# Performance work log

Measured on AMD Instinct MI355X. Metric: run time of the kernel, lower is better.

The kernel has to match this reference:

```python
import jax, jax.numpy as jnp
import numpy as np

N_VOXELS = 200000
DIM = 96
KVOL = 343  # 7^3 depthwise kernel offsets
N_EDGES = 3200000


def setup_inputs() -> dict:
    key = jax.random.key(0)
    ks = jax.random.split(key, 10)
    feats = jax.random.normal(ks[0], (N_VOXELS, DIM), dtype=jnp.float32)
    w_dw = jax.random.normal(ks[1], (KVOL, DIM), dtype=jnp.float32) * 0.02
    b_dw = jax.random.normal(ks[2], (DIM,), dtype=jnp.float32) * 0.02
    ln_w = jnp.ones((DIM,), dtype=jnp.float32)
    ln_b = jnp.zeros((DIM,), dtype=jnp.float32)
    w1 = jax.random.normal(ks[3], (DIM, 4 * DIM), dtype=jnp.float32) * 0.02
    b1 = jax.random.normal(ks[4], (4 * DIM,), dtype=jnp.float32) * 0.02
    w2 = jax.random.normal(ks[5], (4 * DIM, DIM), dtype=jnp.float32) * 0.02
    b2 = jax.random.normal(ks[6], (DIM,), dtype=jnp.float32) * 0.02
    in_idx = jax.random.randint(ks[7], (N_EDGES,), 0, N_VOXELS, dtype=jnp.int32)
    out_idx = jax.random.randint(ks[8], (N_EDGES,), 0, N_VOXELS, dtype=jnp.int32)
    kernel_idx = jax.random.randint(ks[9], (N_EDGES,), 0, KVOL, dtype=jnp.int32)
    return {"feats": feats, "w_dw": w_dw, "b_dw": b_dw, "ln_w": ln_w,
            "ln_b": ln_b, "w1": w1, "b1": b1, "w2": w2, "b2": b2,
            "in_idx": in_idx, "out_idx": out_idx, "kernel_idx": kernel_idx}


def reference(feats, w_dw, b_dw, ln_w, ln_b, w1, b1, w2, b2,
              in_idx, out_idx, kernel_idx):
    n = feats.shape[0]
    # sparse depthwise conv via kernel-map gather/scatter:
    # out[o, c] += feats[i, c] * w_dw[k, c] for each edge (i, o, k)
    contrib = feats[in_idx] * w_dw[kernel_idx]           # [E, C]
    x = jax.ops.segment_sum(contrib, out_idx, num_segments=n) + b_dw
    # LayerNorm over channels, eps=1e-6
    mu = jnp.mean(x, axis=-1, keepdims=True)
    var = jnp.mean(jnp.square(x - mu), axis=-1, keepdims=True)
    x = (x - mu) * jax.lax.rsqrt(var + 1e-6) * ln_w + ln_b
    # pointwise MLP with exact GELU
    h = jax.nn.gelu(x @ w1 + b1, approximate=False)      # [N, 4C]
    x = h @ w2 + b2                                      # [N, C]
    # residual (drop_path rate 0.0 -> identity)
    return feats + x
```

## Files before the change

kernel.cpp:

```cpp
#include <hip/hip_runtime.h>
#include <hip/hip_bf16.h>

#define NVOX 200000
#define DIM 96
#define KVOL 343
#define NEDGE 3200000
#define HID 384
#define TM 32
#define SLOT_CAP 64

typedef __attribute__((ext_vector_type(8))) __bf16 bf16x8;
typedef __attribute__((ext_vector_type(4))) __bf16 bf16x4;
typedef __attribute__((ext_vector_type(4))) float f32x4;

__global__ void prep(const float* __restrict__ feats, const float* __restrict__ w1,
                     const float* __restrict__ w2, const float* __restrict__ w_dw,
                     __bf16* __restrict__ featsb, __hip_bfloat16* __restrict__ w1t,
                     __hip_bfloat16* __restrict__ w2t, __bf16* __restrict__ wdwb,
                     int* __restrict__ cnt) {
    int t = blockIdx.x * 256 + threadIdx.x;
    float4 v = *(const float4*)(feats + t * 4);
    bf16x4 o;
    o[0] = (__bf16)v.x; o[1] = (__bf16)v.y; o[2] = (__bf16)v.z; o[3] = (__bf16)v.w;
    *(bf16x4*)(featsb + t * 4) = o;
    if (t < HID * DIM) {
        int n1 = t / DIM, k1 = t % DIM;
        w1t[t] = __float2bfloat16(w1[k1 * HID + n1]);
        int n2 = t / HID, k2 = t % HID;
        w2t[t] = __float2bfloat16(w2[k2 * DIM + n2]);
        if (t < KVOL * DIM) wdwb[t] = (__bf16)w_dw[t];
    }
    if (t < NVOX) cnt[t] = 0;
}

__global__ void scatter_slots(const int4* __restrict__ in4, const int4* __restrict__ out4,
                              const int4* __restrict__ k4, int* __restrict__ cnt,
                              unsigned* __restrict__ slots) {
    int t = blockIdx.x * 256 + threadIdx.x;
    int4 i = in4[t], o = out4[t], k = k4[t];
    int d;
    d = atomicAdd(&cnt[o.x], 1);
    __builtin_nontemporal_store((unsigned)i.x | ((unsigned)k.x << 18), &slots[o.x * SLOT_CAP + d]);
    d = atomicAdd(&cnt[o.y], 1);
    __builtin_nontemporal_store((unsigned)i.y | ((unsigned)k.y << 18), &slots[o.y * SLOT_CAP + d]);
    d = atomicAdd(&cnt[o.z], 1);
    __builtin_nontemporal_store((unsigned)i.z | ((unsigned)k.z << 18), &slots[o.z * SLOT_CAP + d]);
    d = atomicAdd(&cnt[o.w], 1);
    __builtin_nontemporal_store((unsigned)i.w | ((unsigned)k.w << 18), &slots[o.w * SLOT_CAP + d]);
}

__global__ __launch_bounds__(256, 4) void fused_all(
    const __bf16* __restrict__ featsb, const __bf16* __restrict__ wdwb,
    const float* __restrict__ b_dw,
    const float* __restrict__ ln_w, const float* __restrict__ ln_b,
    const __hip_bfloat16* __restrict__ w1t, const float* __restrict__ b1,
    const __hip_bfloat16* __restrict__ w2t, const float* __restrict__ b2,
    const unsigned* __restrict__ slots, const int* __restrict__ cnt,
    float* __restrict__ out)
{
    __shared__ __hip_bfloat16 At[TM][104];
    __shared__ __align__(16) char shb[TM * 392 * 2];
    __hip_bfloat16 (*Ht)[392] = (__hip_bfloat16 (*)[392])shb;
    unsigned (*recsL)[68] = (unsigned (*)[68])shb;

    const int t   = threadIdx.x;
    const int blk = blockIdx.x;

    {
        const int row  = t >> 3;
        const int sub  = t & 7;
        const int part = sub & 3;
        const int half = sub >> 2;
        const int c0   = part * 24;
        const int v    = blk * TM + row;

        int c = cnt[v];
        if (c > SLOT_CAP) c = SLOT_CAP;
        const unsigned* sp = slots + v * SLOT_CAP;

        if (sub * 4 < c)
            *(uint4*)&recsL[row][sub * 4] = *(const uint4*)(sp + sub * 4);
        if (32 + sub * 4 < c)
            *(uint4*)&recsL[row][32 + sub * 4] = *(const uint4*)(sp + 32 + sub * 4);
        __syncthreads();

        float xa[24];
        #pragma unroll
        for (int j = 0; j < 24; ++j) xa[j] = 0.f;

        const __bf16* fbase = featsb + c0;
        const __bf16* wbase = wdwb + c0;
        const unsigned* rl = recsL[row];

        const int e_lo = half ? (c >> 1) : 0;
        const int e_hi = half ? c : (c >> 1);

#define LDE(F, W, ee) { unsigned rr = rl[ee]; \
        const __bf16* fr = fbase + (int)(rr & 0x3FFFFu) * DIM; \
        const __bf16* wr = wbase + (int)(rr >> 18) * DIM; \
        F##0 = *(const bf16x8*)(fr);      W##0 = *(const bf16x8*)(wr); \
        F##1 = *(const bf16x8*)(fr + 8);  W##1 = *(const bf16x8*)(wr + 8); \
        F##2 = *(const bf16x8*)(fr + 16); W##2 = *(const bf16x8*)(wr + 16); }

#define ACC(F, W) { \
        _Pragma("unroll") for (int j = 0; j < 8; ++j) xa[j]      += (float)F##0[j] * (float)W##0[j]; \
        _Pragma("unroll") for (int j = 0; j < 8; ++j) xa[8 + j]  += (float)F##1[j] * (float)W##1[j]; \
        _Pragma("unroll") for (int j = 0; j < 8; ++j) xa[16 + j] += (float)F##2[j] * (float)W##2[j]; }

        bf16x8 Af0, Af1, Af2, Aw0, Aw1, Aw2, Bf0, Bf1, Bf2, Bw0, Bw1, Bw2;
        int e = e_lo;
        if (e + 2 <= e_hi) {
            LDE(Af, Aw, e); LDE(Bf, Bw, e + 1);
            e += 2;
            for (; e + 2 <= e_hi; e += 2) {
                bf16x8 Cf0, Cf1, Cf2, Cw0, Cw1, Cw2, Df0, Df1, Df2, Dw0, Dw1, Dw2;
                LDE(Cf, Cw, e); LDE(Df, Dw, e + 1);
                ACC(Af, Aw); ACC(Bf, Bw);
                Af0 = Cf0; Af1 = Cf1; Af2 = Cf2; Aw0 = Cw0; Aw1 = Cw1; Aw2 = Cw2;
                Bf0 = Df0; Bf1 = Df1; Bf2 = Df2; Bw0 = Dw0; Bw1 = Dw1; Bw2 = Dw2;
            }
            ACC(Af, Aw); ACC(Bf, Bw);
        }
        if (e < e_hi) {
            LDE(Af, Aw, e);
            ACC(Af, Aw);
        }
#undef LDE
#undef ACC

        #pragma unroll
        for (int j = 0; j < 24; ++j) xa[j] += __shfl_xor(xa[j], 4);

        float s = 0.f, s2 = 0.f;
        #pragma unroll
        for (int j = 0; j < 24; ++j) {
            float x = xa[j] + b_dw[c0 + j];
            xa[j] = x;
            s += x; s2 += x * x;
        }
        s  += __shfl_xor(s, 1);  s  += __shfl_xor(s, 2);
        s2 += __shfl_xor(s2, 1); s2 += __shfl_xor(s2, 2);
        float mean = s * (1.f / 96.f);
        float var  = s2 * (1.f / 96.f) - mean * mean;
        float rstd = rsqrtf(var + 1e-6f);

        if (half == 0) {
            #pragma unroll
            for (int jj = 0; jj < 3; ++jj) {
                bf16x8 pack;
                #pragma unroll
                for (int j = 0; j < 8; ++j) {
                    int cch = c0 + jj*8 + j;
                    float xn = (xa[jj*8+j] - mean) * rstd * ln_w[cch] + ln_b[cch];
                    pack[j] = (__bf16)xn;
                }
                *(bf16x8*)&At[row][c0 + jj*8] = pack;
            }
        }
    }
    __syncthreads();

    const int w  = t >> 6;
    const int l  = t & 63;
    const int lr = l & 15;
    const int lk = l >> 4;
    const int rb = w >> 1;
    const int jh = w & 1;

    f32x4 acc[12];
    #pragma unroll
    for (int j = 0; j < 12; ++j) acc[j] = (f32x4){0.f, 0.f, 0.f, 0.f};

    #pragma unroll
    for (int kk = 0; kk < 3; ++kk) {
        bf16x8 a = *(const bf16x8*)&At[rb*16 + lr][kk*32 + lk*8];
        #pragma unroll
        for (int j = 0; j < 12; ++j) {
            int col = jh*192 + j*16 + lr;
            bf16x8 b = *(const bf16x8*)&w1t[col * DIM + kk*32 + lk*8];
            acc[j] = __builtin_amdgcn_mfma_f32_16x16x32_bf16(a, b, acc[j], 0, 0, 0);
        }
    }

    #pragma unroll
    for (int j = 0; j < 12; ++j) {
        int col = jh*192 + j*16 + lr;
        float bb = b1[col];
        #pragma unroll
        for (int r = 0; r < 4; ++r) {
            float vv = acc[j][r] + bb;
            float ge = 0.5f * vv * (1.f + erff(vv * 0.70710678f));
            Ht[rb*16 + lk*4 + r][col] = __float2bfloat16(ge);
        }
    }
    __syncthreads();

    f32x4 acc2[3];
    #pragma unroll
    for (int j = 0; j < 3; ++j) acc2[j] = (f32x4){0.f, 0.f, 0.f, 0.f};

    #pragma unroll
    for (int kk = 0; kk < 12; ++kk) {
        bf16x8 a = *(const bf16x8*)&Ht[rb*16 + lr][kk*32 + lk*8];
        #pragma unroll
        for (int j = 0; j < 3; ++j) {
            int col = jh*48 + j*16 + lr;
            bf16x8 b = *(const bf16x8*)&w2t[col * HID + kk*32 + lk*8];
            acc2[j] = __builtin_amdgcn_mfma_f32_16x16x32_bf16(a, b, acc2[j], 0, 0, 0);
        }
    }

    #pragma unroll
    for (int j = 0; j < 3; ++j) {
        int col = jh*48 + j*16 + lr;
        float bb = b2[col];
        #pragma unroll
        for (int r = 0; r < 4; ++r) {
            int grow = blk * TM + rb*16 + lk*4 + r;
            int off = grow * DIM + col;
            float res = (float)featsb[off];
            __builtin_nontemporal_store(acc2[j][r] + bb + res, &out[off]);
        }
    }
}

extern "C" void kernel_launch(void* const* d_in, const int* in_sizes, int n_in,
                              void* d_out, int out_size, void* d_ws, size_t ws_size,
                              hipStream_t stream) {
    const float* feats = (const float*)d_in[0];
    const float* w_dw  = (const float*)d_in[1];
    const float* b_dw  = (const float*)d_in[2];
    const float* ln_w  = (const float*)d_in[3];
    const float* ln_b  = (const float*)d_in[4];
    const float* w1    = (const float*)d_in[5];
    const float* b1    = (const float*)d_in[6];
    const float* w2    = (const float*)d_in[7];
    const float* b2    = (const float*)d_in[8];
    const int* in_idx  = (const int*)d_in[9];
    const int* out_idx = (const int*)d_in[10];
    const int* k_idx   = (const int*)d_in[11];
    float* out = (float*)d_out;

    char* ws = (char*)d_ws;
    unsigned* slots = (unsigned*)ws;
    int* cnt   = (int*)(ws + 51200000);
    __hip_bfloat16* w1t = (__hip_bfloat16*)(ws + 52000000);
    __hip_bfloat16* w2t = (__hip_bfloat16*)(ws + 52073728);
    __bf16* wdwb = (__bf16*)(ws + 52147456);
    __bf16* featsb = (__bf16*)(ws + 52213312);

    prep<<<(NVOX * DIM / 4) / 256, 256, 0, stream>>>(feats, w1, w2, w_dw,
                                                     featsb, w1t, w2t, wdwb, cnt);
    scatter_slots<<<NEDGE / 4 / 256, 256, 0, stream>>>((const int4*)in_idx,
                                                       (const int4*)out_idx,
                                                       (const int4*)k_idx, cnt, slots);
    fused_all<<<NVOX / TM, 256, 0, stream>>>(featsb, wdwb, b_dw, ln_w, ln_b,
                                             w1t, b1, w2t, b2, slots, cnt, out);
}
```

Measured before the change: 535.0 us.

## Use 512 threads per block in fused kernel and split edge gather four ways

```diff
diff --git a/kernel.cpp b/kernel.cpp
--- a/kernel.cpp
+++ b/kernel.cpp
@@ -12,6 +12,7 @@
 typedef __attribute__((ext_vector_type(8))) __bf16 bf16x8;
 typedef __attribute__((ext_vector_type(4))) __bf16 bf16x4;
 typedef __attribute__((ext_vector_type(4))) float f32x4;
+typedef __attribute__((ext_vector_type(4))) int i32x4;
 
 __global__ void prep(const float* __restrict__ feats, const float* __restrict__ w1,
                      const float* __restrict__ w2, const float* __restrict__ w_dw,
@@ -19,10 +20,10 @@
                      __hip_bfloat16* __restrict__ w2t, __bf16* __restrict__ wdwb,
                      int* __restrict__ cnt) {
     int t = blockIdx.x * 256 + threadIdx.x;
-    float4 v = *(const float4*)(feats + t * 4);
+    f32x4 v = __builtin_nontemporal_load((const f32x4*)(feats + t * 4));
     bf16x4 o;
     o[0] = (__bf16)v.x; o[1] = (__bf16)v.y; o[2] = (__bf16)v.z; o[3] = (__bf16)v.w;
-    *(bf16x4*)(featsb + t * 4) = o;
+    __builtin_nontemporal_store(o, (bf16x4*)(featsb + t * 4));
     if (t < HID * DIM) {
         int n1 = t / DIM, k1 = t % DIM;
         w1t[t] = __float2bfloat16(w1[k1 * HID + n1]);
@@ -33,23 +34,30 @@
     if (t < NVOX) cnt[t] = 0;
 }
 
-__global__ void scatter_slots(const int4* __restrict__ in4, const int4* __restrict__ out4,
-                              const int4* __restrict__ k4, int* __restrict__ cnt,
+__global__ void scatter_slots(const i32x4* __restrict__ in4, const i32x4* __restrict__ out4,
+                              const i32x4* __restrict__ k4, int* __restrict__ cnt,
                               unsigned* __restrict__ slots) {
     int t = blockIdx.x * 256 + threadIdx.x;
-    int4 i = in4[t], o = out4[t], k = k4[t];
-    int d;
-    d = atomicAdd(&cnt[o.x], 1);
-    __builtin_nontemporal_store((unsigned)i.x | ((unsigned)k.x << 18), &slots[o.x * SLOT_CAP + d]);
-    d = atomicAdd(&cnt[o.y], 1);
-    __builtin_nontemporal_store((unsigned)i.y | ((unsigned)k.y << 18), &slots[o.y * SLOT_CAP + d]);
-    d = atomicAdd(&cnt[o.z], 1);
-    __builtin_nontemporal_store((unsigned)i.z | ((unsigned)k.z << 18), &slots[o.z * SLOT_CAP + d]);
-    d = atomicAdd(&cnt[o.w], 1);
-    __builtin_nontemporal_store((unsigned)i.w | ((unsigned)k.w << 18), &slots[o.w * SLOT_CAP + d]);
-}
-
-__global__ __launch_bounds__(256, 4) void fused_all(
+    if (t >= NEDGE / 8) return;
+    #pragma unroll
+    for (int h = 0; h < 2; ++h) {
+        int idx = t * 2 + h;
+        i32x4 i = __builtin_nontemporal_load(&in4[idx]);
+        i32x4 o = __builtin_nontemporal_load(&out4[idx]);
+        i32x4 k = __builtin_nontemporal_load(&k4[idx]);
+        int d;
+        d = atomicAdd(&cnt[o.x], 1);
+        __builtin_nontemporal_store((unsigned)i.x | ((unsigned)k.x << 18), &slots[o.x * SLOT_CAP + d]);
+        d = atomicAdd(&cnt[o.y], 1);
+        __builtin_nontemporal_store((unsigned)i.y | ((unsigned)k.y << 18), &slots[o.y * SLOT_CAP + d]);
+        d = atomicAdd(&cnt[o.z], 1);
+        __builtin_nontemporal_store((unsigned)i.z | ((unsigned)k.z << 18), &slots[o.z * SLOT_CAP + d]);
+        d = atomicAdd(&cnt[o.w], 1);
+        __builtin_nontemporal_store((unsigned)i.w | ((unsigned)k.w << 18), &slots[o.w * SLOT_CAP + d]);
+    }
+}
+
+__global__ __launch_bounds__(512, 4) void fused_all(
     const __bf16* __restrict__ featsb, const __bf16* __restrict__ wdwb,
     const float* __restrict__ b_dw,
     const float* __restrict__ ln_w, const float* __restrict__ ln_b,
@@ -67,10 +75,10 @@
     const int blk = blockIdx.x;
 
     {
-        const int row  = t >> 3;
-        const int sub  = t & 7;
+        const int row  = t >> 4;
+        const int sub  = t & 15;
         const int part = sub & 3;
-        const int half = sub >> 2;
+        const int q    = sub >> 2;
         const int c0   = part * 24;
         const int v    = blk * TM + row;
 
@@ -80,8 +88,6 @@
 
         if (sub * 4 < c)
             *(uint4*)&recsL[row][sub * 4] = *(const uint4*)(sp + sub * 4);
-        if (32 + sub * 4 < c)
-            *(uint4*)&recsL[row][32 + sub * 4] = *(const uint4*)(sp + 32 + sub * 4);
         __syncthreads();
 
         float xa[24];
@@ -92,8 +98,8 @@
         const __bf16* wbase = wdwb + c0;
         const unsigned* rl = recsL[row];
 
-        const int e_lo = half ? (c >> 1) : 0;
-        const int e_hi = half ? c : (c >> 1);
+        const int e_lo = (c * q) >> 2;
+        const int e_hi = (c * (q + 1)) >> 2;
 
 #define LDE(F, W, ee) { unsigned rr = rl[ee]; \
         const __bf16* fr = fbase + (int)(rr & 0x3FFFFu) * DIM; \
@@ -107,29 +113,25 @@
         _Pragma("unroll") for (int j = 0; j < 8; ++j) xa[8 + j]  += (float)F##1[j] * (float)W##1[j]; \
         _Pragma("unroll") for (int j = 0; j < 8; ++j) xa[16 + j] += (float)F##2[j] * (float)W##2[j]; }
 
-        bf16x8 Af0, Af1, Af2, Aw0, Aw1, Aw2, Bf0, Bf1, Bf2, Bw0, Bw1, Bw2;
-        int e = e_lo;
-        if (e + 2 <= e_hi) {
-            LDE(Af, Aw, e); LDE(Bf, Bw, e + 1);
-            e += 2;
-            for (; e + 2 <= e_hi; e += 2) {
-                bf16x8 Cf0, Cf1, Cf2, Cw0, Cw1, Cw2, Df0, Df1, Df2, Dw0, Dw1, Dw2;
-                LDE(Cf, Cw, e); LDE(Df, Dw, e + 1);
-                ACC(Af, Aw); ACC(Bf, Bw);
-                Af0 = Cf0; Af1 = Cf1; Af2 = Cf2; Aw0 = Cw0; Aw1 = Cw1; Aw2 = Cw2;
-                Bf0 = Df0; Bf1 = Df1; Bf2 = Df2; Bw0 = Dw0; Bw1 = Dw1; Bw2 = Dw2;
-            }
-            ACC(Af, Aw); ACC(Bf, Bw);
-        }
-        if (e < e_hi) {
+        for (int e = e_lo; e < e_hi; e += 3) {
+            int m = e_hi - e;
+            bf16x8 Af0, Af1, Af2, Aw0, Aw1, Aw2;
+            bf16x8 Bf0, Bf1, Bf2, Bw0, Bw1, Bw2;
+            bf16x8 Cf0, Cf1, Cf2, Cw0, Cw1, Cw2;
             LDE(Af, Aw, e);
+            if (m > 1) LDE(Bf, Bw, e + 1);
+            if (m > 2) LDE(Cf, Cw, e + 2);
             ACC(Af, Aw);
+            if (m > 1) ACC(Bf, Bw);
+            if (m > 2) ACC(Cf, Cw);
         }
 #undef LDE
 #undef ACC
 
         #pragma unroll
         for (int j = 0; j < 24; ++j) xa[j] += __shfl_xor(xa[j], 4);
+        #pragma unroll
+        for (int j = 0; j < 24; ++j) xa[j] += __shfl_xor(xa[j], 8);
 
         float s = 0.f, s2 = 0.f;
         #pragma unroll
@@ -144,7 +146,7 @@
         float var  = s2 * (1.f / 96.f) - mean * mean;
         float rstd = rsqrtf(var + 1e-6f);
 
-        if (half == 0) {
+        if (q == 0) {
             #pragma unroll
             for (int jj = 0; jj < 3; ++jj) {
                 bf16x8 pack;
@@ -164,27 +166,27 @@
     const int l  = t & 63;
     const int lr = l & 15;
     const int lk = l >> 4;
-    const int rb = w >> 1;
-    const int jh = w & 1;
-
-    f32x4 acc[12];
-    #pragma unroll
-    for (int j = 0; j < 12; ++j) acc[j] = (f32x4){0.f, 0.f, 0.f, 0.f};
+    const int rb = w >> 2;
+    const int jg = w & 3;
+
+    f32x4 acc[6];
+    #pragma unroll
+    for (int j = 0; j < 6; ++j) acc[j] = (f32x4){0.f, 0.f, 0.f, 0.f};
 
     #pragma unroll
     for (int kk = 0; kk < 3; ++kk) {
         bf16x8 a = *(const bf16x8*)&At[rb*16 + lr][kk*32 + lk*8];
         #pragma unroll
-        for (int j = 0; j < 12; ++j) {
-            int col = jh*192 + j*16 + lr;
+        for (int j = 0; j < 6; ++j) {
+            int col = jg*96 + j*16 + lr;
             bf16x8 b = *(const bf16x8*)&w1t[col * DIM + kk*32 + lk*8];
             acc[j] = __builtin_amdgcn_mfma_f32_16x16x32_bf16(a, b, acc[j], 0, 0, 0);
         }
     }
 
     #pragma unroll
-    for (int j = 0; j < 12; ++j) {
-        int col = jh*192 + j*16 + lr;
+    for (int j = 0; j < 6; ++j) {
+        int col = jg*96 + j*16 + lr;
         float bb = b1[col];
         #pragma unroll
         for (int r = 0; r < 4; ++r) {
@@ -195,24 +197,25 @@
     }
     __syncthreads();
 
-    f32x4 acc2[3];
-    #pragma unroll
-    for (int j = 0; j < 3; ++j) acc2[j] = (f32x4){0.f, 0.f, 0.f, 0.f};
+    const int jt0   = (jg < 2) ? jg * 2 : jg + 2;
+    const int ntile = (jg < 2) ? 2 : 1;
+
+    f32x4 acc2[2];
+    acc2[0] = (f32x4){0.f, 0.f, 0.f, 0.f};
+    acc2[1] = (f32x4){0.f, 0.f, 0.f, 0.f};
 
     #pragma unroll
     for (int kk = 0; kk < 12; ++kk) {
         bf16x8 a = *(const bf16x8*)&Ht[rb*16 + lr][kk*32 + lk*8];
-        #pragma unroll
-        for (int j = 0; j < 3; ++j) {
-            int col = jh*48 + j*16 + lr;
+        for (int j = 0; j < ntile; ++j) {
+            int col = (jt0 + j)*16 + lr;
             bf16x8 b = *(const bf16x8*)&w2t[col * HID + kk*32 + lk*8];
             acc2[j] = __builtin_amdgcn_mfma_f32_16x16x32_bf16(a, b, acc2[j], 0, 0, 0);
         }
     }
 
-    #pragma unroll
-    for (int j = 0; j < 3; ++j) {
-        int col = jh*48 + j*16 + lr;
+    for (int j = 0; j < ntile; ++j) {
+        int col = (jt0 + j)*16 + lr;
         float bb = b2[col];
         #pragma unroll
         for (int r = 0; r < 4; ++r) {
@@ -251,9 +254,9 @@
 
     prep<<<(NVOX * DIM / 4) / 256, 256, 0, stream>>>(feats, w1, w2, w_dw,
                                                      featsb, w1t, w2t, wdwb, cnt);
-    scatter_slots<<<NEDGE / 4 / 256, 256, 0, stream>>>((const int4*)in_idx,
-                                                       (const int4*)out_idx,
-                                                       (const int4*)k_idx, cnt, slots);
-    fused_all<<<NVOX / TM, 256, 0, stream>>>(featsb, wdwb, b_dw, ln_w, ln_b,
+    scatter_slots<<<(NEDGE / 8 + 255) / 256, 256, 0, stream>>>((const i32x4*)in_idx,
+                                                               (const i32x4*)out_idx,
+                                                               (const i32x4*)k_idx, cnt, slots);
+    fused_all<<<NVOX / TM, 512, 0, stream>>>(featsb, wdwb, b_dw, ln_w, ln_b,
                                              w1t, b1, w2t, b2, slots, cnt, out);
 }
```

After: 660.9 us. 23.5% more time.

## Merge prep with edge scatter and split MLP hidden dim to halve LDS

Applied to the files above, without the earlier changes.

```diff
diff --git a/kernel.cpp b/kernel.cpp
--- a/kernel.cpp
+++ b/kernel.cpp
@@ -12,17 +12,25 @@
 typedef __attribute__((ext_vector_type(8))) __bf16 bf16x8;
 typedef __attribute__((ext_vector_type(4))) __bf16 bf16x4;
 typedef __attribute__((ext_vector_type(4))) float f32x4;
-
-__global__ void prep(const float* __restrict__ feats, const float* __restrict__ w1,
-                     const float* __restrict__ w2, const float* __restrict__ w_dw,
-                     __bf16* __restrict__ featsb, __hip_bfloat16* __restrict__ w1t,
-                     __hip_bfloat16* __restrict__ w2t, __bf16* __restrict__ wdwb,
-                     int* __restrict__ cnt) {
+typedef __attribute__((ext_vector_type(4))) int i32x4;
+
+__global__ void zero_cnt(int* __restrict__ cnt) {
+    int i = blockIdx.x * 256 + threadIdx.x;
+    if (i < NVOX) cnt[i] = 0;
+}
+
+__global__ void prep_scatter(const float* __restrict__ feats, const float* __restrict__ w1,
+                             const float* __restrict__ w2, const float* __restrict__ w_dw,
+                             __bf16* __restrict__ featsb, __hip_bfloat16* __restrict__ w1t,
+                             __hip_bfloat16* __restrict__ w2t, __bf16* __restrict__ wdwb,
+                             const i32x4* __restrict__ in4, const i32x4* __restrict__ out4,
+                             const i32x4* __restrict__ k4, int* __restrict__ cnt,
+                             unsigned* __restrict__ slots) {
     int t = blockIdx.x * 256 + threadIdx.x;
-    float4 v = *(const float4*)(feats + t * 4);
+    f32x4 v = __builtin_nontemporal_load((const f32x4*)(feats + t * 4));
     bf16x4 o;
     o[0] = (__bf16)v.x; o[1] = (__bf16)v.y; o[2] = (__bf16)v.z; o[3] = (__bf16)v.w;
-    *(bf16x4*)(featsb + t * 4) = o;
+    __builtin_nontemporal_store(o, (bf16x4*)(featsb + t * 4));
     if (t < HID * DIM) {
         int n1 = t / DIM, k1 = t % DIM;
         w1t[t] = __float2bfloat16(w1[k1 * HID + n1]);
@@ -30,23 +38,20 @@
         w2t[t] = __float2bfloat16(w2[k2 * DIM + n2]);
         if (t < KVOL * DIM) wdwb[t] = (__bf16)w_dw[t];
     }
-    if (t < NVOX) cnt[t] = 0;
-}
-
-__global__ void scatter_slots(const int4* __restrict__ in4, const int4* __restrict__ out4,
-                              const int4* __restrict__ k4, int* __restrict__ cnt,
-                              unsigned* __restrict__ slots) {
-    int t = blockIdx.x * 256 + threadIdx.x;
-    int4 i = in4[t], o = out4[t], k = k4[t];
-    int d;
-    d = atomicAdd(&cnt[o.x], 1);
-    __builtin_nontemporal_store((unsigned)i.x | ((unsigned)k.x << 18), &slots[o.x * SLOT_CAP + d]);
-    d = atomicAdd(&cnt[o.y], 1);
-    __builtin_nontemporal_store((unsigned)i.y | ((unsigned)k.y << 18), &slots[o.y * SLOT_CAP + d]);
-    d = atomicAdd(&cnt[o.z], 1);
-    __builtin_nontemporal_store((unsigned)i.z | ((unsigned)k.z << 18), &slots[o.z * SLOT_CAP + d]);
-    d = atomicAdd(&cnt[o.w], 1);
-    __builtin_nontemporal_store((unsigned)i.w | ((unsigned)k.w << 18), &slots[o.w * SLOT_CAP + d]);
+    if (t < NEDGE / 4) {
+        i32x4 i = __builtin_nontemporal_load(&in4[t]);
+        i32x4 oo = __builtin_nontemporal_load(&out4[t]);
+        i32x4 k = __builtin_nontemporal_load(&k4[t]);
+        int d;
+        d = atomicAdd(&cnt[oo.x], 1);
+        __builtin_nontemporal_store((unsigned)i.x | ((unsigned)k.x << 18), &slots[oo.x * SLOT_CAP + d]);
+        d = atomicAdd(&cnt[oo.y], 1);
+        __builtin_nontemporal_store((unsigned)i.y | ((unsigned)k.y << 18), &slots[oo.y * SLOT_CAP + d]);
+        d = atomicAdd(&cnt[oo.z], 1);
+        __builtin_nontemporal_store((unsigned)i.z | ((unsigned)k.z << 18), &slots[oo.z * SLOT_CAP + d]);
+        d = atomicAdd(&cnt[oo.w], 1);
+        __builtin_nontemporal_store((unsigned)i.w | ((unsigned)k.w << 18), &slots[oo.w * SLOT_CAP + d]);
+    }
 }
 
 __global__ __launch_bounds__(256, 4) void fused_all(
@@ -59,8 +64,8 @@
     float* __restrict__ out)
 {
     __shared__ __hip_bfloat16 At[TM][104];
-    __shared__ __align__(16) char shb[TM * 392 * 2];
-    __hip_bfloat16 (*Ht)[392] = (__hip_bfloat16 (*)[392])shb;
+    __shared__ __align__(16) char shb[TM * 200 * 2];
+    __hip_bfloat16 (*Ht)[200] = (__hip_bfloat16 (*)[200])shb;
     unsigned (*recsL)[68] = (unsigned (*)[68])shb;
 
     const int t   = threadIdx.x;
@@ -167,46 +172,51 @@
     const int rb = w >> 1;
     const int jh = w & 1;
 
-    f32x4 acc[12];
-    #pragma unroll
-    for (int j = 0; j < 12; ++j) acc[j] = (f32x4){0.f, 0.f, 0.f, 0.f};
-
-    #pragma unroll
-    for (int kk = 0; kk < 3; ++kk) {
-        bf16x8 a = *(const bf16x8*)&At[rb*16 + lr][kk*32 + lk*8];
-        #pragma unroll
-        for (int j = 0; j < 12; ++j) {
-            int col = jh*192 + j*16 + lr;
-            bf16x8 b = *(const bf16x8*)&w1t[col * DIM + kk*32 + lk*8];
-            acc[j] = __builtin_amdgcn_mfma_f32_16x16x32_bf16(a, b, acc[j], 0, 0, 0);
-        }
-    }
-
-    #pragma unroll
-    for (int j = 0; j < 12; ++j) {
-        int col = jh*192 + j*16 + lr;
-        float bb = b1[col];
-        #pragma unroll
-        for (int r = 0; r < 4; ++r) {
-            float vv = acc[j][r] + bb;
-            float ge = 0.5f * vv * (1.f + erff(vv * 0.70710678f));
-            Ht[rb*16 + lk*4 + r][col] = __float2bfloat16(ge);
-        }
-    }
-    __syncthreads();
-
     f32x4 acc2[3];
     #pragma unroll
     for (int j = 0; j < 3; ++j) acc2[j] = (f32x4){0.f, 0.f, 0.f, 0.f};
 
     #pragma unroll
-    for (int kk = 0; kk < 12; ++kk) {
-        bf16x8 a = *(const bf16x8*)&Ht[rb*16 + lr][kk*32 + lk*8];
-        #pragma unroll
-        for (int j = 0; j < 3; ++j) {
-            int col = jh*48 + j*16 + lr;
-            bf16x8 b = *(const bf16x8*)&w2t[col * HID + kk*32 + lk*8];
-            acc2[j] = __builtin_amdgcn_mfma_f32_16x16x32_bf16(a, b, acc2[j], 0, 0, 0);
+    for (int h = 0; h < 2; ++h) {
+        f32x4 acc[6];
+        #pragma unroll
+        for (int j = 0; j < 6; ++j) acc[j] = (f32x4){0.f, 0.f, 0.f, 0.f};
+
+        #pragma unroll
+        for (int kk = 0; kk < 3; ++kk) {
+            bf16x8 a = *(const bf16x8*)&At[rb*16 + lr][kk*32 + lk*8];
+            #pragma unroll
+            for (int j = 0; j < 6; ++j) {
+                int col = h*192 + jh*96 + j*16 + lr;
+                bf16x8 b = *(const bf16x8*)&w1t[col * DIM + kk*32 + lk*8];
+                acc[j] = __builtin_amdgcn_mfma_f32_16x16x32_bf16(a, b, acc[j], 0, 0, 0);
+            }
+        }
+
+        if (h == 1) __syncthreads();
+
+        #pragma unroll
+        for (int j = 0; j < 6; ++j) {
+            int col = h*192 + jh*96 + j*16 + lr;
+            float bb = b1[col];
+            #pragma unroll
+            for (int r = 0; r < 4; ++r) {
+                float vv = acc[j][r] + bb;
+                float ge = 0.5f * vv * (1.f + erff(vv * 0.70710678f));
+                Ht[rb*16 + lk*4 + r][jh*96 + j*16 + lr] = __float2bfloat16(ge);
+            }
+        }
+        __syncthreads();
+
+        #pragma unroll
+        for (int kk = 0; kk < 6; ++kk) {
+            bf16x8 a = *(const bf16x8*)&Ht[rb*16 + lr][kk*32 + lk*8];
+            #pragma unroll
+            for (int j = 0; j < 3; ++j) {
+                int col = jh*48 + j*16 + lr;
+                bf16x8 b = *(const bf16x8*)&w2t[col * HID + (h*6 + kk)*32 + lk*8];
+                acc2[j] = __builtin_amdgcn_mfma_f32_16x16x32_bf16(a, b, acc2[j], 0, 0, 0);
+            }
         }
     }
 
@@ -249,11 +259,10 @@
     __bf16* wdwb = (__bf16*)(ws + 52147456);
     __bf16* featsb = (__bf16*)(ws + 52213312);
 
-    prep<<<(NVOX * DIM / 4) / 256, 256, 0, stream>>>(feats, w1, w2, w_dw,
-                                                     featsb, w1t, w2t, wdwb, cnt);
-    scatter_slots<<<NEDGE / 4 / 256, 256, 0, stream>>>((const int4*)in_idx,
-                                                       (const int4*)out_idx,
-                                                       (const int4*)k_idx, cnt, slots);
+    zero_cnt<<<(NVOX + 255) / 256, 256, 0, stream>>>(cnt);
+    prep_scatter<<<(NVOX * DIM / 4) / 256, 256, 0, stream>>>(
+        feats, w1, w2, w_dw, featsb, w1t, w2t, wdwb,
+        (const i32x4*)in_idx, (const i32x4*)out_idx, (const i32x4*)k_idx, cnt, slots);
     fused_all<<<NVOX / TM, 256, 0, stream>>>(featsb, wdwb, b_dw, ln_w, ln_b,
                                              w1t, b1, w2t, b2, slots, cnt, out);
 }
```

New measurement: 545.0 us. No clear change (+1.9%).
